# Performance work log

Measured on AMD Instinct MI355X. Metric: run time of the kernel, lower is better.

## Reference

```python
import jax, jax.numpy as jnp
import numpy as np

B, L, D, H, K = 1, 1024, 512, 8, 24
h = D // H
EPS = 1e-5


def setup_inputs() -> dict:
    key = jax.random.key(0)
    ks = jax.random.split(key, 8)
    s = 0.02
    return {
        "x": jax.random.normal(ks[0], (B, L, D), jnp.float32),
        "Wq": jax.random.normal(ks[1], (D, D), jnp.float32) * s,
        "bq": jnp.zeros((D,), jnp.float32),
        "Wk": jax.random.normal(ks[2], (D, D), jnp.float32) * s,
        "bk": jnp.zeros((D,), jnp.float32),
        "Wv": jax.random.normal(ks[3], (D, D), jnp.float32) * s,
        "bv": jnp.zeros((D,), jnp.float32),
        "Wo": jax.random.normal(ks[4], (D, D), jnp.float32) * s,
        "bo": jnp.zeros((D,), jnp.float32),
        "Wg": jax.random.normal(ks[5], (h * h, 1), jnp.float32) * s,
        "bg": jnp.zeros((1,), jnp.float32),
        "kv_norm_scale": jnp.ones((1, H, 1, h, h), jnp.float32),
        "qk_norm_scale": jnp.full((1, H, 1), 1.0 / np.sqrt(h), jnp.float32),
        "spectral_filters": jax.random.normal(ks[6], (L, K), jnp.float32) * 0.1,
    }


def _full_conv(filters, u, n_fft, L_out):
    # filters: [L, K], u: [B, H, L, h] -> causal FFT conv: [B, H, L, K, h]
    Ff = jnp.fft.rfft(filters, n=n_fft, axis=0)            # [F, K]
    U = jnp.fft.rfft(u, n=n_fft, axis=2)                    # [B, H, F, h]
    y = jnp.fft.irfft(U[:, :, :, None, :] * Ff[None, None, :, :, None], n=n_fft, axis=2)
    return y[:, :, :L_out]


def reference(x, Wq, bq, Wk, bk, Wv, bv, Wo, bo, Wg, bg,
              kv_norm_scale, qk_norm_scale, spectral_filters):
    Bb, Ll, Dd = x.shape
    q = (x @ Wq + bq).reshape(Bb, Ll, H, h).transpose(0, 2, 1, 3)  # [B,H,L,h]
    k = (x @ Wk + bk).reshape(Bb, Ll, H, h).transpose(0, 2, 1, 3)
    v = (x @ Wv + bv).reshape(Bb, Ll, H, h).transpose(0, 2, 1, 3)

    sim = jnp.einsum("bhld,bhld->bhl", q, k) * qk_norm_scale       # [B,H,L]

    # F.normalize(dim=-1)
    k = k / jnp.maximum(jnp.linalg.norm(k, axis=-1, keepdims=True), 1e-12)
    v = v / jnp.maximum(jnp.linalg.norm(v, axis=-1, keepdims=True), 1e-12)

    n_fft = 2 * Ll
    k = _full_conv(spectral_filters, k, n_fft, Ll)  # [B,H,L,K,h]
    v = _full_conv(spectral_filters, v, n_fft, Ll)

    Z = jnp.einsum("bhlkd,bhlke->bhlde", v, k) * kv_norm_scale     # [B,H,L,h,h]

    logits = Z.reshape(Bb, H, Ll, h * h) @ Wg + bg                  # [B,H,L,1]
    gates = jax.nn.relu(logits) ** 2 + EPS
    gates = gates[..., None]                                        # [B,H,L,1,1]
    gated_Z = gates * Z

    # Online-softmax associative scan over L for (m, s); Z/g combine is pure add -> cumsum.
    def combine(a, b):
        m_x, s_x = a
        m_y, s_y = b
        m = jnp.maximum(m_x, m_y)
        return (m, s_x * jnp.exp(m_x - m) + s_y * jnp.exp(m_y - m))

    m_scan, s_scan = jax.lax.associative_scan(combine, (sim, jnp.ones_like(sim)), axis=2)
    Z_scan = jnp.cumsum(gated_Z, axis=2)
    g_scan = jnp.cumsum(gates, axis=2)

    softmax_w = jnp.exp(sim - m_scan)[..., None, None] / (s_scan[..., None, None] + EPS)
    gated_w = Z_scan / (g_scan + EPS)
    attn = gated_w * (1.0 + jax.nn.silu(softmax_w))                 # [B,H,L,h,h]

    ctxt = jnp.einsum("bhld,bhlde->bhle", q, attn)                  # [B,H,L,h]
    ctxt = ctxt.transpose(0, 2, 1, 3).reshape(Bb, Ll, Dd)
    return ctxt @ Wo + bo
```

## Files before the change

### kernel.cpp

```cpp
#include <hip/hip_runtime.h>
#include <math.h>

#define Hh 8
#define Ll 1024
#define KF 24
#define Dm 512
#define EPSf 1e-5f
#define LK (Ll*KF)

typedef __attribute__((ext_vector_type(8))) short sh8;
typedef __attribute__((ext_vector_type(4))) short sh4;
typedef __attribute__((ext_vector_type(4))) float f32x4;

#define OFF_QH     0
#define OFF_KN     524288
#define OFF_VN     1048576
#define OFF_SIM    1572864
#define OFF_LOGITS 1581056
#define OFF_GATES  1589248
#define OFF_FACTOR 1597440
#define OFF_VCB    1605632
#define OFF_KCB    7897088
#define OFF_QPK    14188544
#define OFF_MPK    14450688
#define OFF_WOPK   14467072
#define OFF_CPK    14598144
#define OFF_CZP    26771456
#define OFF_S0     28868608
#define OFF_CPART  29392896
#define OFF_FPK_F  26771456
#define OFF_UPK_F  27607040
#define OFF_APK_F  28131328
#define OFF_BPK_F  28393472

__device__ inline unsigned short f2bf(float x){
    unsigned int u = __float_as_uint(x);
    unsigned int r = (u + 0x7fffu + ((u>>16)&1u)) >> 16;
    return (unsigned short)r;
}
__device__ inline float bf2f(unsigned short u){ return __uint_as_float(((unsigned int)u)<<16); }
__device__ inline sh8 ld8_8B(const unsigned short* p){
    union { sh8 s; sh4 h[2]; } u;
    u.h[0] = *(const sh4*)(p);
    u.h[1] = *(const sh4*)(p+4);
    return u.s;
}

__global__ __launch_bounds__(256) void pack_all_kernel(
    const float* __restrict__ x,
    const float* __restrict__ Wq, const float* __restrict__ Wk, const float* __restrict__ Wv,
    const float* __restrict__ Wo, const float* __restrict__ kvs, const float* __restrict__ Wg,
    const float* __restrict__ filt,
    unsigned short* __restrict__ Apk, unsigned short* __restrict__ Bpk,
    unsigned short* __restrict__ Wopk, unsigned short* __restrict__ Mpk,
    unsigned short* __restrict__ Fpk16)
{
    int bid = blockIdx.x, tid = threadIdx.x;
    if (bid < 64){
        int mb = bid;
        for (int ks=0; ks<16; ks++){
            #pragma unroll
            for (int p=0;p<2;p++){
                int e = tid + p*256;
                int lane = e>>3, j = e&7;
                int m = mb*16 + (lane&15);
                int k = ks*32 + ((lane>>4)&3)*8 + j;
                Apk[(mb*16+ks)*512 + e] = f2bf(x[m*Dm + k]);
            }
        }
    } else if (bid < 160){
        int nb = bid - 64;
        int n0 = nb*16;
        int mm = n0>>9;
        const float* W = (mm==0)?Wq:((mm==1)?Wk:Wv);
        int coff = n0 & 511;
        for (int ks=0; ks<16; ks++){
            #pragma unroll
            for (int p=0;p<2;p++){
                int e = tid + p*256;
                int lane = e>>3, j = e&7;
                int kk = ks*32 + ((lane>>4)&3)*8 + j;
                Bpk[(nb*16+ks)*512 + e] = f2bf(W[kk*Dm + coff + (lane&15)]);
            }
        }
    } else if (bid < 192){
        int nb = bid - 160;
        int n0 = nb*16;
        for (int ks=0; ks<16; ks++){
            #pragma unroll
            for (int p=0;p<2;p++){
                int e = tid + p*256;
                int lane = e>>3, j = e&7;
                int kk = ks*32 + ((lane>>4)&3)*8 + j;
                Wopk[(nb*16+ks)*512 + e] = f2bf(Wo[kk*Dm + n0 + (lane&15)]);
            }
        }
    } else if (bid < 200){
        int hd = bid - 192;
        for (int it=0; it<16; it++){
            int idx = tid + it*256;
            int f = idx & 511, ksnb = idx >> 9;
            int nb = ksnb>>1, ks = ksnb&1;
            int lane = f>>3, j = f&7;
            int e = nb*16 + (lane&15);
            int d = ks*32 + ((lane>>4)&3)*8 + j;
            Mpk[hd*4096 + idx] = f2bf(kvs[(hd*64+e)*64 + d]*Wg[e*64+d]);
        }
    } else {
        int b2 = bid - 200;
        for (int ti=0; ti<16; ti++){
            int tile = b2*16 + ti;
            int kf = tile>>6, d16 = tile&63;
            unsigned short* dst = Fpk16 + tile*1024;
            #pragma unroll
            for (int p2=0;p2<4;p2++){
                int e = tid + p2*256;
                int ks = e>>9, f = e&511;
                int lane = f>>3, j = f&7;
                int m = lane&15;
                int k = ks*32 + ((lane>>4)&3)*8 + j;
                int fidx = 16*d16 + m - k;
                float v = (fidx>=0 && fidx<Ll) ? filt[fidx*KF+kf] : 0.0f;
                dst[e] = f2bf(v);
            }
        }
    }
}

__global__ __launch_bounds__(256) void qkvm_kernel(
    const unsigned short* __restrict__ Apk, const unsigned short* __restrict__ Bpk,
    const float* __restrict__ bq, const float* __restrict__ bk, const float* __restrict__ bv,
    float* __restrict__ qh, float* __restrict__ kn, float* __restrict__ vn)
{
    int mt = blockIdx.x, nt = blockIdx.y;
    int tid = threadIdx.x, wid = tid>>6, lane = tid&63;
    int mb = mt*4 + wid;
    f32x4 acc[4];
    #pragma unroll
    for (int nb=0;nb<4;nb++) acc[nb]=(f32x4){0.f,0.f,0.f,0.f};
    for (int ks=0; ks<16; ks++){
        sh8 a = *(const sh8*)(Apk + (mb*16+ks)*512 + lane*8);
        #pragma unroll
        for (int nb2=0;nb2<4;nb2++){
            sh8 b = *(const sh8*)(Bpk + ((nt*4+nb2)*16+ks)*512 + lane*8);
            acc[nb2] = __builtin_amdgcn_mfma_f32_16x16x32_bf16(a, b, acc[nb2], 0,0,0);
        }
    }
    int mm = nt>>3, hd = nt&7;
    const float* bias = (mm==0)?bq:((mm==1)?bk:bv);
    float* dst = (mm==0)?qh:((mm==1)?kn:vn);
    int quad = lane>>4, col = lane&15;
    #pragma unroll
    for (int nb2=0;nb2<4;nb2++){
        int d = nb2*16 + col;
        float bval = bias[hd*64+d];
        #pragma unroll
        for (int r=0;r<4;r++){
            int t = mb*16 + quad*4 + r;
            dst[(hd*Ll + t)*64 + d] = acc[nb2][r] + bval;
        }
    }
}

__global__ __launch_bounds__(256) void nse_kernel(
    const float* __restrict__ qh, const float* __restrict__ kn, const float* __restrict__ vn,
    const float* __restrict__ qks, float* __restrict__ simg,
    unsigned short* __restrict__ Upk, unsigned short* __restrict__ Qpk)
{
    int gw = blockIdx.x*4 + (threadIdx.x>>6);
    int lane = threadIdx.x & 63;
    int hd = gw>>10, t = gw&1023;
    int base = gw*64 + lane;
    float q = qh[base], k = kn[base], v = vn[base];
    float sim = q*k, k2 = k*k, v2 = v*v;
    #pragma unroll
    for (int off=32; off; off>>=1){
        sim += __shfl_xor(sim, off, 64);
        k2  += __shfl_xor(k2,  off, 64);
        v2  += __shfl_xor(v2,  off, 64);
    }
    float kfv = k * (1.f/fmaxf(sqrtf(k2), 1e-12f));
    float vfv = v * (1.f/fmaxf(sqrtf(v2), 1e-12f));
    int d = lane;
    int ST = t>>6, ks = (t>>5)&1, j = t&7;
    int frag = ks*2048 + (d>>4)*512 + (((t>>3)&3)*16 + (d&15))*8 + j;
    Upk[((hd*16) + ST)*4096 + frag]        = f2bf(vfv);
    Upk[(((8+hd)*16) + ST)*4096 + frag]    = f2bf(kfv);
    int mb = t>>4, ks2 = d>>5, j2 = d&7;
    int fl2 = ((d>>3)&3)*16 + (t&15);
    Qpk[((hd*64+mb)*2+ks2)*512 + fl2*8 + j2] = f2bf(q);
    if (lane==0) simg[gw] = sim * qks[hd];
}

__device__ __forceinline__ void conv_phase(
    int T, int kf0, int hd,
    const unsigned short* __restrict__ Fpk16,
    const unsigned short* __restrict__ Uv, const unsigned short* __restrict__ Uk,
    const unsigned short* __restrict__ Mh,
    unsigned short* __restrict__ vcb, unsigned short* __restrict__ kcb,
    float* __restrict__ logits, unsigned short* lds,
    int tid, int w, int lane)
{
    int quad = lane>>4, lm = lane&15;
    f32x4 acc[2][2][4];
    #pragma unroll
    for (int kf=0;kf<2;kf++)
        #pragma unroll
        for (int tz=0;tz<2;tz++)
            #pragma unroll
            for (int nb=0;nb<4;nb++) acc[kf][tz][nb]=(f32x4){0.f,0.f,0.f,0.f};

    __syncthreads();
    {
        sh8 v0=*(const sh8*)(Uv+tid*8), v1=*(const sh8*)(Uv+(tid+256)*8);
        sh8 k0=*(const sh8*)(Uk+tid*8), k1=*(const sh8*)(Uk+(tid+256)*8);
        *(sh8*)(&lds[tid*8])=v0; *(sh8*)(&lds[(tid+256)*8])=v1;
        *(sh8*)(&lds[4096+tid*8])=k0; *(sh8*)(&lds[4096+(tid+256)*8])=k1;
    }
    for (int ST=0; ST<=T; ST++){
        sh8 nv0,nv1,nk0,nk1;
        bool more = (ST < T);
        if (more){
            const unsigned short* Uvn = Uv + (ST+1)*4096;
            const unsigned short* Ukn = Uk + (ST+1)*4096;
            nv0=*(const sh8*)(Uvn+tid*8); nv1=*(const sh8*)(Uvn+(tid+256)*8);
            nk0=*(const sh8*)(Ukn+tid*8); nk1=*(const sh8*)(Ukn+(tid+256)*8);
        }
        int d16 = 4*(T-ST) + w;
        sh8 a[2][2];
        #pragma unroll
        for (int kf=0;kf<2;kf++)
            #pragma unroll
            for (int ks=0;ks<2;ks++)
                a[kf][ks] = *(const sh8*)(Fpk16 + ((kf0+kf)*64 + d16)*1024 + ks*512 + lane*8);
        __syncthreads();
        const unsigned short* Bb = &lds[(ST&1)*8192];
        #pragma unroll
        for (int ks=0;ks<2;ks++)
            #pragma unroll
            for (int nb=0;nb<4;nb++){
                sh8 bv = *(const sh8*)(Bb + ks*2048 + nb*512 + lane*8);
                sh8 bk = *(const sh8*)(Bb + 4096 + ks*2048 + nb*512 + lane*8);
                #pragma unroll
                for (int kf=0;kf<2;kf++){
                    acc[kf][0][nb] = __builtin_amdgcn_mfma_f32_16x16x32_bf16(
                        a[kf][ks], bv, acc[kf][0][nb], 0,0,0);
                    acc[kf][1][nb] = __builtin_amdgcn_mfma_f32_16x16x32_bf16(
                        a[kf][ks], bk, acc[kf][1][nb], 0,0,0);
                }
            }
        if (more){
            unsigned short* Bn = &lds[((ST+1)&1)*8192];
            *(sh8*)(Bn+tid*8)=nv0; *(sh8*)(Bn+(tid+256)*8)=nv1;
            *(sh8*)(Bn+4096+tid*8)=nk0; *(sh8*)(Bn+4096+(tid+256)*8)=nk1;
        }
    }
    float logacc[4] = {0.f,0.f,0.f,0.f};
    #pragma unroll
    for (int kf=0;kf<2;kf++){
        __syncthreads();
        #pragma unroll
        for (int tz=0;tz<2;tz++)
            #pragma unroll
            for (int nb=0;nb<4;nb++)
                #pragma unroll
                for (int r=0;r<4;r++){
                    int tl = w*16 + quad*4 + r;
                    lds[tz*4608 + tl*72 + nb*16 + lm] = f2bf(acc[kf][tz][nb][r]);
                }
        __syncthreads();
        #pragma unroll
        for (int tz=0;tz<2;tz++){
            unsigned short* dst = tz ? kcb : vcb;
            #pragma unroll
            for (int it=0; it<2; it++){
                int idx = tid + it*256;
                int row = idx>>3, seg = idx&7;
                sh8 vv = *(const sh8*)(&lds[tz*4608 + row*72 + seg*8]);
                *(sh8*)(dst + ((hd*Ll + T*64 + row)*KF + kf0+kf)*64 + seg*8) = vv;
            }
        }
        f32x4 accp[4];
        #pragma unroll
        for (int nb=0;nb<4;nb++) accp[nb]=(f32x4){0.f,0.f,0.f,0.f};
        #pragma unroll
        for (int ks=0;ks<2;ks++){
            sh8 a2 = *(const sh8*)(&lds[4608 + (w*16+lm)*72 + ks*32 + quad*8]);
            #pragma unroll
            for (int nb=0;nb<4;nb++){
                sh8 bm = *(const sh8*)(Mh + (nb*2+ks)*512 + lane*8);
                accp[nb] = __builtin_amdgcn_mfma_f32_16x16x32_bf16(a2, bm, accp[nb], 0,0,0);
            }
        }
        #pragma unroll
        for (int r=0;r<4;r++){
            int rloc = w*16 + quad*4 + r;
            float s = 0.f;
            #pragma unroll
            for (int nb=0;nb<4;nb++)
                s += accp[nb][r]*bf2f(lds[rloc*72 + nb*16 + lm]);
            logacc[r] += s;
        }
    }
    #pragma unroll
    for (int r=0;r<4;r++){
        float s = logacc[r];
        s += __shfl_xor(s, 1, 64);
        s += __shfl_xor(s, 2, 64);
        s += __shfl_xor(s, 4, 64);
        s += __shfl_xor(s, 8, 64);
        if (lm==0)
            atomicAdd(&logits[hd*Ll + T*64 + w*16 + quad*4 + r], s);
    }
}

__global__ __launch_bounds__(256,2) void convf_kernel(
    const unsigned short* __restrict__ Fpk16, const unsigned short* __restrict__ Upk,
    const unsigned short* __restrict__ Mpk,
    unsigned short* __restrict__ vcb, unsigned short* __restrict__ kcb,
    float* __restrict__ logits)
{
    __shared__ unsigned short lds[16384];
    int p = blockIdx.x, kf0 = blockIdx.y*2, hd = blockIdx.z;
    int tid=threadIdx.x, w=tid>>6, lane=tid&63;
    const unsigned short* Uv = Upk + (hd*16)*4096;
    const unsigned short* Uk = Upk + ((8+hd)*16)*4096;
    const unsigned short* Mh = Mpk + hd*4096;
    conv_phase(15-p, kf0, hd, Fpk16, Uv, Uk, Mh, vcb, kcb, logits, lds, tid, w, lane);
    conv_phase(p,    kf0, hd, Fpk16, Uv, Uk, Mh, vcb, kcb, logits, lds, tid, w, lane);
}

__global__ __launch_bounds__(256) void scan_kernel(
    const float* __restrict__ simg, const float* __restrict__ logits,
    const float* __restrict__ bg, float* __restrict__ gates, float* __restrict__ factor)
{
    int hd=blockIdx.x, tid=threadIdx.x;
    __shared__ float sm[256], ssc[256], sg[256];
    float bgv = bg[0];
    float simv[4], m_loc[4], s_loc[4], g_loc[4];
    float m = -__builtin_inff(), s = 0.f, g = 0.f;
    for(int e=0;e<4;e++){
        int ix = hd*Ll + tid*4 + e;
        simv[e] = simg[ix];
        float lg = logits[ix] + bgv;
        float r = fmaxf(lg, 0.f);
        float gv = r*r + EPSf;
        gates[ix] = gv;
        float mn = fmaxf(m, simv[e]);
        s = s*__expf(m-mn) + __expf(simv[e]-mn);
        m = mn; g += gv;
        m_loc[e]=m; s_loc[e]=s; g_loc[e]=g;
    }
    sm[tid]=m; ssc[tid]=s; sg[tid]=g;
    __syncthreads();
    for(int off=1; off<256; off<<=1){
        float pm=0, ps=0, pg=0; bool has = (tid>=off);
        if(has){ pm=sm[tid-off]; ps=ssc[tid-off]; pg=sg[tid-off]; }
        __syncthreads();
        if(has){
            float mn=fmaxf(pm, sm[tid]);
            float sn=ps*__expf(pm-mn) + ssc[tid]*__expf(sm[tid]-mn);
            sm[tid]=mn; ssc[tid]=sn; sg[tid]=pg+sg[tid];
        }
        __syncthreads();
    }
    float pm=-__builtin_inff(), ps=0.f, pg=0.f;
    if (tid>0){ pm=sm[tid-1]; ps=ssc[tid-1]; pg=sg[tid-1]; }
    for(int e=0;e<4;e++){
        float mn=fmaxf(pm, m_loc[e]);
        float sn=ps*__expf(pm-mn) + s_loc[e]*__expf(m_loc[e]-mn);
        float gn=pg + g_loc[e];
        float sw = __expf(simv[e]-mn)/(sn+EPSf);
        float silu = sw/(1.f+__expf(-sw));
        factor[hd*Ll + tid*4 + e] = (1.f+silu)/(gn+EPSf);
    }
}

#define VTS 68
#define ASS 72
__global__ __launch_bounds__(256) void p3cz_kernel(
    const unsigned short* __restrict__ Qpk,
    const unsigned short* __restrict__ vcb, const unsigned short* __restrict__ kcb,
    const float* __restrict__ gates, float* __restrict__ cpart, float* __restrict__ czp)
{
    __shared__ unsigned short VT[64*VTS];
    __shared__ unsigned short KT[64*VTS];
    __shared__ unsigned short As[4][16*ASS];
    __shared__ unsigned short Vraw[64*72];
    __shared__ float gl[16];
    int tid=threadIdx.x, w=tid>>6, lane=tid&63;
    int quad=lane>>4, lm=lane&15;
    int c=blockIdx.x, qq=blockIdx.y, hd=blockIdx.z;
    int T0=c*64, tq0=T0+qq*16, RQ0=tq0*KF;
    if (tid<16) gl[tid]=gates[hd*Ll+tq0+tid];
    sh8 aq[2];
    {
        const unsigned short* qb = Qpk + ((hd*64 + (c*4+w))*2)*512;
        aq[0] = *(const sh8*)(qb + lane*8);
        aq[1] = *(const sh8*)(qb + 512 + lane*8);
    }
    f32x4 ctx[4], cz[4];
    #pragma unroll
    for (int nb=0;nb<4;nb++){ ctx[nb]=(f32x4){0,0,0,0}; cz[nb]=(f32x4){0,0,0,0}; }
    int t_g = T0 + w*16 + quad*4;
    int rp = tid>>3, e0 = (tid&7)*8, r0 = rp*2;

    for (int sub=0; sub<6; sub++){
        int RB = RQ0 + sub*64;
        const unsigned short* vrow = vcb + (hd*LK + RB)*64;
        const unsigned short* krow = kcb + (hd*LK + RB)*64;
        __syncthreads();
        {
            float g0 = gl[(RB + r0)/KF - tq0];
            float g1 = gl[(RB + r0 + 1)/KF - tq0];
            sh8 v0 = *(const sh8*)(vrow + r0*64 + e0);
            sh8 v1 = *(const sh8*)(vrow + (r0+1)*64 + e0);
            sh8 k0 = *(const sh8*)(krow + r0*64 + e0);
            sh8 k1 = *(const sh8*)(krow + (r0+1)*64 + e0);
            *(sh8*)(&Vraw[r0*72 + e0]) = v0;
            *(sh8*)(&Vraw[(r0+1)*72 + e0]) = v1;
            #pragma unroll
            for (int j=0;j<8;j++){
                unsigned int pv = (unsigned int)f2bf(bf2f((unsigned short)v0[j])*g0)
                                | ((unsigned int)f2bf(bf2f((unsigned short)v1[j])*g1)<<16);
                *(unsigned int*)(&VT[(e0+j)*VTS + r0]) = pv;
                unsigned int pk = (unsigned int)(unsigned short)k0[j]
                                | ((unsigned int)(unsigned short)k1[j]<<16);
                *(unsigned int*)(&KT[(e0+j)*VTS + r0]) = pk;
            }
        }
        __syncthreads();
        f32x4 S[4];
        #pragma unroll
        for (int nb=0;nb<4;nb++) S[nb]=(f32x4){0,0,0,0};
        #pragma unroll
        for (int ks=0;ks<2;ks++){
            #pragma unroll
            for (int nb=0;nb<4;nb++){
                sh8 b = *(const sh8*)(&Vraw[(nb*16+lm)*72 + ks*32 + quad*8]);
                S[nb] = __builtin_amdgcn_mfma_f32_16x16x32_bf16(aq[ks], b, S[nb], 0,0,0);
            }
        }
        #pragma unroll
        for (int nb=0;nb<4;nb++){
            int row_l = nb*16+lm;
            int tp = (RB + row_l)/KF;
            float g = gl[tp - tq0];
            #pragma unroll
            for (int r=0;r<4;r++){
                float v = (t_g + r >= tp) ? S[nb][r]*g : 0.f;
                As[w][(quad*4+r)*ASS + row_l] = f2bf(v);
            }
        }
        #pragma unroll
        for (int ks=0;ks<2;ks++){
            sh8 a2 = *(const sh8*)(&As[w][lm*ASS + ks*32 + quad*8]);
            sh8 av = ld8_8B(&VT[(w*16+lm)*VTS + ks*32 + quad*8]);
            #pragma unroll
            for (int nb=0;nb<4;nb++){
                sh8 bk = ld8_8B(&KT[(nb*16+lm)*VTS + ks*32 + quad*8]);
                ctx[nb] = __builtin_amdgcn_mfma_f32_16x16x32_bf16(a2, bk, ctx[nb], 0,0,0);
                cz[nb]  = __builtin_amdgcn_mfma_f32_16x16x32_bf16(av, bk, cz[nb], 0,0,0);
            }
        }
    }
    #pragma unroll
    for (int nb=0;nb<4;nb++){
        #pragma unroll
        for (int r=0;r<4;r++){
            cpart[((qq*8+hd)*Ll + t_g + r)*64 + nb*16+lm] = ctx[nb][r];
        }
    }
    int ob = ((hd*16+c)*4+qq)*4096;
    #pragma unroll
    for (int nb=0;nb<4;nb++){
        #pragma unroll
        for (int r=0;r<4;r++){
            czp[ob + (w*16+quad*4+r)*64 + nb*16+lm] = cz[nb][r];
        }
    }
}

__global__ __launch_bounds__(256) void s0_kernel(
    const float* __restrict__ czp, unsigned short* __restrict__ S0b)
{
    int idx = blockIdx.x*256 + threadIdx.x;
    int hd = blockIdx.y;
    int d = idx>>6, e = idx&63;
    int frag = (d>>5)*2048 + (e>>4)*512 + ((((d>>3)&3)*16) + (e&15))*8 + (d&7);
    float a = 0.f;
    for (int c=0;c<16;c++){
        S0b[(hd*16+c)*4096 + frag] = f2bf(a);
        int b = ((hd*16+c)*4)*4096 + idx;
        a += czp[b] + czp[b+4096] + czp[b+2*4096] + czp[b+3*4096];
    }
}

__global__ __launch_bounds__(256) void combine_kernel(
    const unsigned short* __restrict__ Qpk, const unsigned short* __restrict__ S0b,
    const float* __restrict__ cpart, const float* __restrict__ factor,
    unsigned short* __restrict__ Cpk)
{
    int c=blockIdx.x, hd=blockIdx.y;
    int tid=threadIdx.x, wid=tid>>6, lane=tid&63, quad=lane>>4, lm=lane&15;
    int mb = c*4 + wid;
    sh8 aq0 = *(const sh8*)(Qpk + ((hd*64+mb)*2)*512 + lane*8);
    sh8 aq1 = *(const sh8*)(Qpk + ((hd*64+mb)*2+1)*512 + lane*8);
    const unsigned short* sb = S0b + (hd*16+c)*4096;
    f32x4 acc[4];
    #pragma unroll
    for (int nb=0;nb<4;nb++) acc[nb]=(f32x4){0.f,0.f,0.f,0.f};
    #pragma unroll
    for (int ks=0;ks<2;ks++){
        sh8 a = ks ? aq1 : aq0;
        #pragma unroll
        for (int nb=0;nb<4;nb++){
            sh8 b = *(const sh8*)(sb + ks*2048 + nb*512 + lane*8);
            acc[nb] = __builtin_amdgcn_mfma_f32_16x16x32_bf16(a, b, acc[nb], 0,0,0);
        }
    }
    float fv[4];
    #pragma unroll
    for (int r=0;r<4;r++) fv[r] = factor[hd*Ll + mb*16 + quad*4 + r];
    #pragma unroll
    for (int nb=0;nb<4;nb++){
        int e = nb*16 + lm;
        int dim = hd*64 + e;
        int ks2 = dim>>5, koff = dim&31, qd = koff>>3, jj = koff&7;
        #pragma unroll
        for (int r=0;r<4;r++){
            int t = mb*16 + quad*4 + r;
            float v = acc[nb][r];
            #pragma unroll
            for (int q=0;q<4;q++) v += cpart[((q*8+hd)*Ll + t)*64 + e];
            v *= fv[r];
            Cpk[((t>>4)*16 + ks2)*512 + qd*128 + (t&15)*8 + jj] = f2bf(v);
        }
    }
}

__global__ __launch_bounds__(256) void outprojm_kernel(
    const unsigned short* __restrict__ Cpk, const unsigned short* __restrict__ Wopk,
    const float* __restrict__ bo, float* __restrict__ out)
{
    int mt=blockIdx.x, nt=blockIdx.y;
    int tid=threadIdx.x, wid=tid>>6, lane=tid&63;
    int mb=mt*4+wid;
    f32x4 acc[4];
    #pragma unroll
    for (int nb=0;nb<4;nb++) acc[nb]=(f32x4){0.f,0.f,0.f,0.f};
    for (int ks=0;ks<16;ks++){
        sh8 a = *(const sh8*)(Cpk + (mb*16+ks)*512 + lane*8);
        #pragma unroll
        for (int nb2=0;nb2<4;nb2++){
            sh8 b = *(const sh8*)(Wopk + ((nt*4+nb2)*16+ks)*512 + lane*8);
            acc[nb2] = __builtin_amdgcn_mfma_f32_16x16x32_bf16(a, b, acc[nb2], 0,0,0);
        }
    }
    int quad=lane>>4, col=lane&15;
    #pragma unroll
    for (int nb2=0;nb2<4;nb2++){
        int n = nt*64 + nb2*16 + col;
        float bval = bo[n];
        #pragma unroll
        for (int r=0;r<4;r++){
            out[(mb*16+quad*4+r)*Dm + n] = acc[nb2][r] + bval;
        }
    }
}

extern "C" void kernel_launch(void* const* d_in, const int* in_sizes, int n_in,
                              void* d_out, int out_size, void* d_ws, size_t ws_size,
                              hipStream_t stream)
{
    (void)in_sizes; (void)n_in; (void)out_size; (void)ws_size;
    const float* x   =(const float*)d_in[0];
    const float* Wq  =(const float*)d_in[1];
    const float* bq  =(const float*)d_in[2];
    const float* Wk  =(const float*)d_in[3];
    const float* bk  =(const float*)d_in[4];
    const float* Wv  =(const float*)d_in[5];
    const float* bv  =(const float*)d_in[6];
    const float* Wo  =(const float*)d_in[7];
    const float* bo  =(const float*)d_in[8];
    const float* Wg  =(const float*)d_in[9];
    const float* bg  =(const float*)d_in[10];
    const float* kvs =(const float*)d_in[11];
    const float* qks =(const float*)d_in[12];
    const float* filt=(const float*)d_in[13];
    float* ws = (float*)d_ws;
    float* qh    = ws+OFF_QH;
    float* kn    = ws+OFF_KN;
    float* vn    = ws+OFF_VN;
    float* simg  = ws+OFF_SIM;
    float* logits= ws+OFF_LOGITS;
    float* gates = ws+OFF_GATES;
    float* factor= ws+OFF_FACTOR;
    float* czp   = ws+OFF_CZP;
    float* cpart = ws+OFF_CPART;
    unsigned short* vcb  = (unsigned short*)(ws + OFF_VCB);
    unsigned short* kcb  = (unsigned short*)(ws + OFF_KCB);
    unsigned short* Qpk  = (unsigned short*)(ws + OFF_QPK);
    unsigned short* Mpk  = (unsigned short*)(ws + OFF_MPK);
    unsigned short* Wopk = (unsigned short*)(ws + OFF_WOPK);
    unsigned short* Cpk  = (unsigned short*)(ws + OFF_CPK);
    unsigned short* S0b  = (unsigned short*)(ws + OFF_S0);
    unsigned short* Fpk16= (unsigned short*)(ws + OFF_FPK_F);
    unsigned short* Upk  = (unsigned short*)(ws + OFF_UPK_F);
    unsigned short* Apk  = (unsigned short*)(ws + OFF_APK_F);
    unsigned short* Bpk  = (unsigned short*)(ws + OFF_BPK_F);
    float* out   = (float*)d_out;

    hipMemsetAsync(logits, 0, Hh*Ll*sizeof(float), stream);
    pack_all_kernel<<<dim3(296),    256,0,stream>>>(x,Wq,Wk,Wv,Wo,kvs,Wg,filt,
                                                    Apk,Bpk,Wopk,Mpk,Fpk16);
    qkvm_kernel   <<<dim3(16,24),   256,0,stream>>>(Apk,Bpk,bq,bk,bv,qh,kn,vn);
    nse_kernel    <<<dim3(2048),    256,0,stream>>>(qh,kn,vn,qks,simg,Upk,Qpk);
    convf_kernel  <<<dim3(8,12,8),  256,0,stream>>>(Fpk16,Upk,Mpk,vcb,kcb,logits);
    scan_kernel   <<<dim3(8),       256,0,stream>>>(simg,logits,bg,gates,factor);
    p3cz_kernel   <<<dim3(16,4,8),  256,0,stream>>>(Qpk,vcb,kcb,gates,cpart,czp);
    s0_kernel     <<<dim3(16,8),    256,0,stream>>>(czp,S0b);
    combine_kernel<<<dim3(16,8),    256,0,stream>>>(Qpk,S0b,cpart,factor,Cpk);
    outprojm_kernel<<<dim3(16,8),   256,0,stream>>>(Cpk,Wopk,bo,out);
}
```

Baseline: 175.6 us.

## Fuse QKV projection with normalization, fold memset into pack, prefetch p3cz loads

Merges the QKV GEMM and the norm/sim/pack kernel into one per-head kernel, so each 16-row tile computes q, k and v together and does the reductions in registers. This removes the fp32 qh/kn/vn round trip through global memory and one launch. The logits memset moves into an extra block of the pack kernel. p3cz now software-prefetches the next sub-tile's v/k rows, the czp partials are stored as bf16, and convf's occupancy hint rises to 3. The bf16 partials add rounding to the prefix sums, and the fused GEMM launches small 64-thread blocks.

```diff
diff --git a/kernel.cpp b/kernel.cpp
--- a/kernel.cpp
+++ b/kernel.cpp
@@ -12,9 +12,6 @@
 typedef __attribute__((ext_vector_type(4))) short sh4;
 typedef __attribute__((ext_vector_type(4))) float f32x4;
 
-#define OFF_QH     0
-#define OFF_KN     524288
-#define OFF_VN     1048576
 #define OFF_SIM    1572864
 #define OFF_LOGITS 1581056
 #define OFF_GATES  1589248
@@ -53,7 +50,7 @@
     const float* __restrict__ filt,
     unsigned short* __restrict__ Apk, unsigned short* __restrict__ Bpk,
     unsigned short* __restrict__ Wopk, unsigned short* __restrict__ Mpk,
-    unsigned short* __restrict__ Fpk16)
+    unsigned short* __restrict__ Fpk16, float* __restrict__ logits)
 {
     int bid = blockIdx.x, tid = threadIdx.x;
     if (bid < 64){
@@ -106,7 +103,7 @@
             int d = ks*32 + ((lane>>4)&3)*8 + j;
             Mpk[hd*4096 + idx] = f2bf(kvs[(hd*64+e)*64 + d]*Wg[e*64+d]);
         }
-    } else {
+    } else if (bid < 296){
         int b2 = bid - 200;
         for (int ti=0; ti<16; ti++){
             int tile = b2*16 + ti;
@@ -124,72 +121,80 @@
                 dst[e] = f2bf(v);
             }
         }
-    }
-}
-
-__global__ __launch_bounds__(256) void qkvm_kernel(
+    } else {
+        for (int i=tid; i<Hh*Ll; i+=256) logits[i] = 0.f;
+    }
+}
+
+__global__ __launch_bounds__(64) void qkvn_kernel(
     const unsigned short* __restrict__ Apk, const unsigned short* __restrict__ Bpk,
     const float* __restrict__ bq, const float* __restrict__ bk, const float* __restrict__ bv,
-    float* __restrict__ qh, float* __restrict__ kn, float* __restrict__ vn)
-{
-    int mt = blockIdx.x, nt = blockIdx.y;
-    int tid = threadIdx.x, wid = tid>>6, lane = tid&63;
-    int mb = mt*4 + wid;
-    f32x4 acc[4];
-    #pragma unroll
-    for (int nb=0;nb<4;nb++) acc[nb]=(f32x4){0.f,0.f,0.f,0.f};
+    const float* __restrict__ qks, float* __restrict__ simg,
+    unsigned short* __restrict__ Upk, unsigned short* __restrict__ Qpk)
+{
+    int mb = blockIdx.x, hd = blockIdx.y;
+    int lane = threadIdx.x, quad = lane>>4, lm = lane&15;
+    f32x4 acc[3][4];
+    #pragma unroll
+    for (int mm=0;mm<3;mm++)
+        #pragma unroll
+        for (int nbl=0;nbl<4;nbl++) acc[mm][nbl]=(f32x4){0.f,0.f,0.f,0.f};
     for (int ks=0; ks<16; ks++){
         sh8 a = *(const sh8*)(Apk + (mb*16+ks)*512 + lane*8);
         #pragma unroll
-        for (int nb2=0;nb2<4;nb2++){
-            sh8 b = *(const sh8*)(Bpk + ((nt*4+nb2)*16+ks)*512 + lane*8);
-            acc[nb2] = __builtin_amdgcn_mfma_f32_16x16x32_bf16(a, b, acc[nb2], 0,0,0);
-        }
-    }
-    int mm = nt>>3, hd = nt&7;
-    const float* bias = (mm==0)?bq:((mm==1)?bk:bv);
-    float* dst = (mm==0)?qh:((mm==1)?kn:vn);
-    int quad = lane>>4, col = lane&15;
-    #pragma unroll
-    for (int nb2=0;nb2<4;nb2++){
-        int d = nb2*16 + col;
-        float bval = bias[hd*64+d];
+        for (int mm=0;mm<3;mm++)
+            #pragma unroll
+            for (int nbl=0;nbl<4;nbl++){
+                sh8 b = *(const sh8*)(Bpk + ((mm*32 + hd*4 + nbl)*16 + ks)*512 + lane*8);
+                acc[mm][nbl] = __builtin_amdgcn_mfma_f32_16x16x32_bf16(a, b, acc[mm][nbl], 0,0,0);
+            }
+    }
+    #pragma unroll
+    for (int nbl=0;nbl<4;nbl++){
+        float bqv = bq[hd*64 + nbl*16 + lm];
+        float bkv = bk[hd*64 + nbl*16 + lm];
+        float bvv = bv[hd*64 + nbl*16 + lm];
         #pragma unroll
         for (int r=0;r<4;r++){
-            int t = mb*16 + quad*4 + r;
-            dst[(hd*Ll + t)*64 + d] = acc[nb2][r] + bval;
-        }
-    }
-}
-
-__global__ __launch_bounds__(256) void nse_kernel(
-    const float* __restrict__ qh, const float* __restrict__ kn, const float* __restrict__ vn,
-    const float* __restrict__ qks, float* __restrict__ simg,
-    unsigned short* __restrict__ Upk, unsigned short* __restrict__ Qpk)
-{
-    int gw = blockIdx.x*4 + (threadIdx.x>>6);
-    int lane = threadIdx.x & 63;
-    int hd = gw>>10, t = gw&1023;
-    int base = gw*64 + lane;
-    float q = qh[base], k = kn[base], v = vn[base];
-    float sim = q*k, k2 = k*k, v2 = v*v;
-    #pragma unroll
-    for (int off=32; off; off>>=1){
-        sim += __shfl_xor(sim, off, 64);
-        k2  += __shfl_xor(k2,  off, 64);
-        v2  += __shfl_xor(v2,  off, 64);
-    }
-    float kfv = k * (1.f/fmaxf(sqrtf(k2), 1e-12f));
-    float vfv = v * (1.f/fmaxf(sqrtf(v2), 1e-12f));
-    int d = lane;
-    int ST = t>>6, ks = (t>>5)&1, j = t&7;
-    int frag = ks*2048 + (d>>4)*512 + (((t>>3)&3)*16 + (d&15))*8 + j;
-    Upk[((hd*16) + ST)*4096 + frag]        = f2bf(vfv);
-    Upk[(((8+hd)*16) + ST)*4096 + frag]    = f2bf(kfv);
-    int mb = t>>4, ks2 = d>>5, j2 = d&7;
-    int fl2 = ((d>>3)&3)*16 + (t&15);
-    Qpk[((hd*64+mb)*2+ks2)*512 + fl2*8 + j2] = f2bf(q);
-    if (lane==0) simg[gw] = sim * qks[hd];
+            acc[0][nbl][r] += bqv; acc[1][nbl][r] += bkv; acc[2][nbl][r] += bvv;
+        }
+    }
+    float simr[4], k2r[4], v2r[4];
+    #pragma unroll
+    for (int r=0;r<4;r++){
+        float ps=0.f, pk=0.f, pv=0.f;
+        #pragma unroll
+        for (int nbl=0;nbl<4;nbl++){
+            float qv=acc[0][nbl][r], kv=acc[1][nbl][r], vv=acc[2][nbl][r];
+            ps += qv*kv; pk += kv*kv; pv += vv*vv;
+        }
+        #pragma unroll
+        for (int off=1; off<16; off<<=1){
+            ps += __shfl_xor(ps, off, 64);
+            pk += __shfl_xor(pk, off, 64);
+            pv += __shfl_xor(pv, off, 64);
+        }
+        simr[r]=ps; k2r[r]=pk; v2r[r]=pv;
+    }
+    float qksv = qks[hd];
+    #pragma unroll
+    for (int r=0;r<4;r++){
+        int t = mb*16 + quad*4 + r;
+        float invk = 1.f/fmaxf(sqrtf(k2r[r]), 1e-12f);
+        float invv = 1.f/fmaxf(sqrtf(v2r[r]), 1e-12f);
+        int ST = t>>6, ksb = (t>>5)&1, j = t&7;
+        int rowf = ((t>>3)&3)*16 + lm;
+        #pragma unroll
+        for (int nbl=0;nbl<4;nbl++){
+            int frag = ksb*2048 + nbl*512 + rowf*8 + j;
+            Upk[((hd*16)+ST)*4096 + frag]     = f2bf(acc[2][nbl][r]*invv);
+            Upk[(((8+hd)*16)+ST)*4096 + frag] = f2bf(acc[1][nbl][r]*invk);
+            int d = nbl*16 + lm;
+            int ks2 = d>>5, j2 = d&7, fl2 = ((d>>3)&3)*16 + (t&15);
+            Qpk[((hd*64+mb)*2+ks2)*512 + fl2*8 + j2] = f2bf(acc[0][nbl][r]);
+        }
+        if (lm==0) simg[hd*Ll + t] = simr[r]*qksv;
+    }
 }
 
 __device__ __forceinline__ void conv_phase(
@@ -314,7 +319,7 @@
     }
 }
 
-__global__ __launch_bounds__(256,2) void convf_kernel(
+__global__ __launch_bounds__(256,3) void convf_kernel(
     const unsigned short* __restrict__ Fpk16, const unsigned short* __restrict__ Upk,
     const unsigned short* __restrict__ Mpk,
     unsigned short* __restrict__ vcb, unsigned short* __restrict__ kcb,
@@ -381,7 +386,8 @@
 __global__ __launch_bounds__(256) void p3cz_kernel(
     const unsigned short* __restrict__ Qpk,
     const unsigned short* __restrict__ vcb, const unsigned short* __restrict__ kcb,
-    const float* __restrict__ gates, float* __restrict__ cpart, float* __restrict__ czp)
+    const float* __restrict__ gates, float* __restrict__ cpart,
+    unsigned short* __restrict__ czp)
 {
     __shared__ unsigned short VT[64*VTS];
     __shared__ unsigned short KT[64*VTS];
@@ -405,29 +411,40 @@
     int t_g = T0 + w*16 + quad*4;
     int rp = tid>>3, e0 = (tid&7)*8, r0 = rp*2;
 
+    sh8 pv0, pv1, pk0, pk1;
+    {
+        const unsigned short* vrow = vcb + (hd*LK + RQ0)*64;
+        const unsigned short* krow = kcb + (hd*LK + RQ0)*64;
+        pv0 = *(const sh8*)(vrow + r0*64 + e0);
+        pv1 = *(const sh8*)(vrow + (r0+1)*64 + e0);
+        pk0 = *(const sh8*)(krow + r0*64 + e0);
+        pk1 = *(const sh8*)(krow + (r0+1)*64 + e0);
+    }
     for (int sub=0; sub<6; sub++){
         int RB = RQ0 + sub*64;
-        const unsigned short* vrow = vcb + (hd*LK + RB)*64;
-        const unsigned short* krow = kcb + (hd*LK + RB)*64;
         __syncthreads();
         {
             float g0 = gl[(RB + r0)/KF - tq0];
             float g1 = gl[(RB + r0 + 1)/KF - tq0];
-            sh8 v0 = *(const sh8*)(vrow + r0*64 + e0);
-            sh8 v1 = *(const sh8*)(vrow + (r0+1)*64 + e0);
-            sh8 k0 = *(const sh8*)(krow + r0*64 + e0);
-            sh8 k1 = *(const sh8*)(krow + (r0+1)*64 + e0);
-            *(sh8*)(&Vraw[r0*72 + e0]) = v0;
-            *(sh8*)(&Vraw[(r0+1)*72 + e0]) = v1;
+            *(sh8*)(&Vraw[r0*72 + e0]) = pv0;
+            *(sh8*)(&Vraw[(r0+1)*72 + e0]) = pv1;
             #pragma unroll
             for (int j=0;j<8;j++){
-                unsigned int pv = (unsigned int)f2bf(bf2f((unsigned short)v0[j])*g0)
-                                | ((unsigned int)f2bf(bf2f((unsigned short)v1[j])*g1)<<16);
+                unsigned int pv = (unsigned int)f2bf(bf2f((unsigned short)pv0[j])*g0)
+                                | ((unsigned int)f2bf(bf2f((unsigned short)pv1[j])*g1)<<16);
                 *(unsigned int*)(&VT[(e0+j)*VTS + r0]) = pv;
-                unsigned int pk = (unsigned int)(unsigned short)k0[j]
-                                | ((unsigned int)(unsigned short)k1[j]<<16);
+                unsigned int pk = (unsigned int)(unsigned short)pk0[j]
+                                | ((unsigned int)(unsigned short)pk1[j]<<16);
                 *(unsigned int*)(&KT[(e0+j)*VTS + r0]) = pk;
             }
+        }
+        if (sub < 5){
+            const unsigned short* vrow = vcb + (hd*LK + RB + 64)*64;
+            const unsigned short* krow = kcb + (hd*LK + RB + 64)*64;
+            pv0 = *(const sh8*)(vrow + r0*64 + e0);
+            pv1 = *(const sh8*)(vrow + (r0+1)*64 + e0);
+            pk0 = *(const sh8*)(krow + r0*64 + e0);
+            pk1 = *(const sh8*)(krow + (r0+1)*64 + e0);
         }
         __syncthreads();
         f32x4 S[4];
@@ -476,13 +493,13 @@
     for (int nb=0;nb<4;nb++){
         #pragma unroll
         for (int r=0;r<4;r++){
-            czp[ob + (w*16+quad*4+r)*64 + nb*16+lm] = cz[nb][r];
+            czp[ob + (w*16+quad*4+r)*64 + nb*16+lm] = f2bf(cz[nb][r]);
         }
     }
 }
 
 __global__ __launch_bounds__(256) void s0_kernel(
-    const float* __restrict__ czp, unsigned short* __restrict__ S0b)
+    const unsigned short* __restrict__ czp, unsigned short* __restrict__ S0b)
 {
     int idx = blockIdx.x*256 + threadIdx.x;
     int hd = blockIdx.y;
@@ -492,7 +509,7 @@
     for (int c=0;c<16;c++){
         S0b[(hd*16+c)*4096 + frag] = f2bf(a);
         int b = ((hd*16+c)*4)*4096 + idx;
-        a += czp[b] + czp[b+4096] + czp[b+2*4096] + czp[b+3*4096];
+        a += bf2f(czp[b]) + bf2f(czp[b+4096]) + bf2f(czp[b+2*4096]) + bf2f(czp[b+3*4096]);
     }
 }
 
@@ -589,14 +606,10 @@
     const float* qks =(const float*)d_in[12];
     const float* filt=(const float*)d_in[13];
     float* ws = (float*)d_ws;
-    float* qh    = ws+OFF_QH;
-    float* kn    = ws+OFF_KN;
-    float* vn    = ws+OFF_VN;
     float* simg  = ws+OFF_SIM;
     float* logits= ws+OFF_LOGITS;
     float* gates = ws+OFF_GATES;
     float* factor= ws+OFF_FACTOR;
-    float* czp   = ws+OFF_CZP;
     float* cpart = ws+OFF_CPART;
     unsigned short* vcb  = (unsigned short*)(ws + OFF_VCB);
     unsigned short* kcb  = (unsigned short*)(ws + OFF_KCB);
@@ -604,6 +617,7 @@
     unsigned short* Mpk  = (unsigned short*)(ws + OFF_MPK);
     unsigned short* Wopk = (unsigned short*)(ws + OFF_WOPK);
     unsigned short* Cpk  = (unsigned short*)(ws + OFF_CPK);
+    unsigned short* czp  = (unsigned short*)(ws + OFF_CZP);
     unsigned short* S0b  = (unsigned short*)(ws + OFF_S0);
     unsigned short* Fpk16= (unsigned short*)(ws + OFF_FPK_F);
     unsigned short* Upk  = (unsigned short*)(ws + OFF_UPK_F);
@@ -611,11 +625,9 @@
     unsigned short* Bpk  = (unsigned short*)(ws + OFF_BPK_F);
     float* out   = (float*)d_out;
 
-    hipMemsetAsync(logits, 0, Hh*Ll*sizeof(float), stream);
-    pack_all_kernel<<<dim3(296),    256,0,stream>>>(x,Wq,Wk,Wv,Wo,kvs,Wg,filt,
-                                                    Apk,Bpk,Wopk,Mpk,Fpk16);
-    qkvm_kernel   <<<dim3(16,24),   256,0,stream>>>(Apk,Bpk,bq,bk,bv,qh,kn,vn);
-    nse_kernel    <<<dim3(2048),    256,0,stream>>>(qh,kn,vn,qks,simg,Upk,Qpk);
+    pack_all_kernel<<<dim3(297),    256,0,stream>>>(x,Wq,Wk,Wv,Wo,kvs,Wg,filt,
+                                                    Apk,Bpk,Wopk,Mpk,Fpk16,logits);
+    qkvn_kernel   <<<dim3(64,8),    64, 0,stream>>>(Apk,Bpk,bq,bk,bv,qks,simg,Upk,Qpk);
     convf_kernel  <<<dim3(8,12,8),  256,0,stream>>>(Fpk16,Upk,Mpk,vcb,kcb,logits);
     scan_kernel   <<<dim3(8),       256,0,stream>>>(simg,logits,bg,gates,factor);
     p3cz_kernel   <<<dim3(16,4,8),  256,0,stream>>>(Qpk,vcb,kcb,gates,cpart,czp);
```

Result: no change. 176.0 us (+0.2%).
